# Kernel optimization log

Hardware: AMD Instinct MI355X
Metric: run time of the kernel (lower is better)

Reference implementation:

```python
import jax, jax.numpy as jnp
import numpy as np

N = 16384          # num_nodes
B = 2              # batch_size
F = 32             # feature_size (hard-coded in module)
G = 16             # num_gru_units
OUT = 16           # output_dim


def _normalized_laplacian(adj):
    # calculate_laplacian_with_self_loop: D^-1/2 (A + I) D^-1/2
    a = adj + jnp.eye(adj.shape[0], dtype=adj.dtype)
    d = a.sum(axis=1)
    dinv = jax.lax.rsqrt(d)
    return dinv[:, None] * a * dinv[None, :]


def setup_inputs() -> dict:
    key = jax.random.key(0)
    k1, k2, k3, k4 = jax.random.split(key, 4)
    adj = (jax.random.uniform(k1, (N, N), dtype=jnp.float32) < 0.01).astype(jnp.float32)
    laplacian = _normalized_laplacian(adj)
    inputs = jax.random.normal(k2, (B, N, F), dtype=jnp.float32)
    hidden_state = jax.random.normal(k3, (B, N * G), dtype=jnp.float32)
    # xavier_uniform for weights [(G+F), OUT]
    limit = np.sqrt(6.0 / (G + F + OUT)).astype(np.float32)
    weights = jax.random.uniform(k4, (G + F, OUT), dtype=jnp.float32, minval=-limit, maxval=limit)
    biases = jnp.zeros((OUT,), dtype=jnp.float32)
    return {"inputs": inputs, "hidden_state": hidden_state, "laplacian": laplacian,
            "weights": weights, "biases": biases}


def reference(inputs, hidden_state, laplacian, weights, biases):
    b, n, f = inputs.shape
    g = weights.shape[0] - f
    out_dim = weights.shape[1]
    h = hidden_state.reshape(b, n, g)
    cat = jnp.concatenate([inputs, h], axis=2)              # [B, N, F+G]
    # laplacian @ concat over the node dimension (same math as the
    # reshape/transpose dance + per-batch sparse GEMM loop in the original)
    ax = jnp.einsum('mn,bnc->bmc', laplacian, cat)          # [B, N, F+G]
    out = ax @ weights + biases                             # [B, N, OUT]
    return out.reshape(b, n * out_dim)
```

## Files before the change

### kernel.cpp

```cpp
#include <hip/hip_runtime.h>
#include <hip/hip_bf16.h>


#define NN   16384
#define FF   32
#define GG   16
#define OUTD 16
#define C96  96
#define BM   64
#define BK   64
#define SPLITK 2
#define KCHUNK (NN / SPLITK)
#define KITERS (KCHUNK / BK)

typedef __attribute__((ext_vector_type(8))) short short8;
typedef __attribute__((ext_vector_type(4))) float f32x4;

using as1_void = __attribute__((address_space(1))) void;
using as3_void = __attribute__((address_space(3))) void;

__device__ __forceinline__ unsigned short f2bf(float f) {
  __hip_bfloat16 h = __float2bfloat16(f);
  return __builtin_bit_cast(unsigned short, h);
}

__device__ __forceinline__ void wg_barrier() {
  asm volatile("" ::: "memory");
  __builtin_amdgcn_s_barrier();
  asm volatile("" ::: "memory");
}

__global__ __launch_bounds__(256) void prep_xt(const float* __restrict__ inp,
                                               const float* __restrict__ hid,
                                               unsigned short* __restrict__ xt) {
  __shared__ float lds_cat[C96][64];
  const int tid = threadIdx.x;
  const int n0 = blockIdx.x * 64;

#pragma unroll
  for (int r = 0; r < 2; ++r) {
    int fi = tid + r * 256;
    int n = fi >> 3;
    int f4 = fi & 7;
#pragma unroll
    for (int b = 0; b < 2; ++b) {
      const float4* src = (const float4*)(inp + ((size_t)b * NN + (n0 + n)) * FF) + f4;
      float4 v = *src;
      int c = b * 48 + f4 * 4;
      lds_cat[c + 0][n] = v.x;
      lds_cat[c + 1][n] = v.y;
      lds_cat[c + 2][n] = v.z;
      lds_cat[c + 3][n] = v.w;
    }
  }
  {
    int n = tid >> 2;
    int g4 = tid & 3;
#pragma unroll
    for (int b = 0; b < 2; ++b) {
      const float4* src = (const float4*)(hid + ((size_t)b * NN + (n0 + n)) * GG) + g4;
      float4 v = *src;
      int c = b * 48 + 32 + g4 * 4;
      lds_cat[c + 0][n] = v.x;
      lds_cat[c + 1][n] = v.y;
      lds_cat[c + 2][n] = v.z;
      lds_cat[c + 3][n] = v.w;
    }
  }
  __syncthreads();
#pragma unroll
  for (int r = 0; r < 3; ++r) {
    int u = tid + r * 256;
    int c = u >> 3;
    int nn = (u & 7) * 8;
    short8 o;
#pragma unroll
    for (int j = 0; j < 8; ++j) o[j] = (short)f2bf(lds_cat[c][nn + j]);
    *(short8*)(xt + (size_t)c * NN + n0 + nn) = o;
  }
}

__global__ __launch_bounds__(256, 2) void spmm_main(const float* __restrict__ L,
                                                    const unsigned short* __restrict__ xt,
                                                    float* __restrict__ cp) {
  __shared__ __align__(16) float lds_a[2][BM * BK];
  __shared__ __align__(16) unsigned short lds_b[2][C96 * BK];

  const int tid = threadIdx.x;
  const int wave = tid >> 6;
  const int lane = tid & 63;

  const int wg = blockIdx.x;
  const int swz = (wg & 7) * (512 / 8) + (wg >> 3);
  const int my = swz >> 8;
  const int mx = swz & 255;
  const int m0 = mx * BM;
  const int kbase = my * KCHUNK;

  const float* asrc[4];
  int adst[4];
#pragma unroll
  for (int a = 0; a < 4; ++a) {
    int s = wave * 256 + a * 64 + lane;
    int row = s >> 4;
    int cu = (s & 15) ^ (row & 15);
    asrc[a] = L + (size_t)(m0 + row) * NN + kbase + cu * 4;
    adst[a] = (wave * 256 + a * 64) * 4;
  }
  const unsigned short* bsrc[3];
  int bdst[3];
#pragma unroll
  for (int bi = 0; bi < 3; ++bi) {
    int s = wave * 192 + bi * 64 + lane;
    int c = s >> 3;
    int kg = (s & 7) ^ (c & 7);
    bsrc[bi] = xt + (size_t)c * NN + kbase + kg * 8;
    bdst[bi] = (wave * 192 + bi * 64) * 8;
  }

  const int rowA = wave * 16 + (lane & 15);
  const int lq = lane >> 4;
  int aoff[2][2];
#pragma unroll
  for (int kk = 0; kk < 2; ++kk) {
    int cu0 = kk * 8 + lq * 2;
    aoff[kk][0] = (rowA * 16 + (cu0 ^ (rowA & 15))) * 4;
    aoff[kk][1] = (rowA * 16 + ((cu0 + 1) ^ (rowA & 15))) * 4;
  }
  int boff[2][6];
#pragma unroll
  for (int kk = 0; kk < 2; ++kk)
#pragma unroll
    for (int t = 0; t < 6; ++t) {
      int c = t * 16 + (lane & 15);
      int kg = kk * 4 + lq;
      boff[kk][t] = (c * 8 + (kg ^ (c & 7))) * 8;
    }

  f32x4 acc[6];
#pragma unroll
  for (int t = 0; t < 6; ++t) acc[t] = (f32x4){0.f, 0.f, 0.f, 0.f};

  auto stage = [&](int buf, int ko) {
#pragma unroll
    for (int a = 0; a < 4; ++a)
      __builtin_amdgcn_global_load_lds((const as1_void*)(asrc[a] + ko),
                                       (as3_void*)(&lds_a[buf][adst[a]]), 16, 0, 0);
#pragma unroll
    for (int bi = 0; bi < 3; ++bi)
      __builtin_amdgcn_global_load_lds((const as1_void*)(bsrc[bi] + ko),
                                       (as3_void*)(&lds_b[buf][bdst[bi]]), 16, 0, 0);
  };

  auto compute = [&](int buf) {
#pragma unroll
    for (int kk = 0; kk < 2; ++kk) {
      f32x4 a0 = *(const f32x4*)(&lds_a[buf][aoff[kk][0]]);
      f32x4 a1 = *(const f32x4*)(&lds_a[buf][aoff[kk][1]]);
      short8 af;
      af[0] = (short)f2bf(a0[0]);
      af[1] = (short)f2bf(a0[1]);
      af[2] = (short)f2bf(a0[2]);
      af[3] = (short)f2bf(a0[3]);
      af[4] = (short)f2bf(a1[0]);
      af[5] = (short)f2bf(a1[1]);
      af[6] = (short)f2bf(a1[2]);
      af[7] = (short)f2bf(a1[3]);
#pragma unroll
      for (int t = 0; t < 6; ++t) {
        short8 bf = *(const short8*)(&lds_b[buf][boff[kk][t]]);
        acc[t] = __builtin_amdgcn_mfma_f32_16x16x32_bf16(af, bf, acc[t], 0, 0, 0);
      }
    }
  };

  stage(0, 0);
  int cur = 0;
  for (int it = 0; it < KITERS - 1; ++it) {
    stage(cur ^ 1, (it + 1) * BK);
    asm volatile("s_waitcnt vmcnt(7)" ::: "memory");
    __builtin_amdgcn_s_barrier();
    asm volatile("" ::: "memory");
    compute(cur);
    wg_barrier();
    cur ^= 1;
  }
  asm volatile("s_waitcnt vmcnt(0)" ::: "memory");
  __builtin_amdgcn_s_barrier();
  asm volatile("" ::: "memory");
  compute(cur);

  float* cpd = cp + ((size_t)my * NN + m0) * C96;
#pragma unroll
  for (int t = 0; t < 6; ++t) {
    int col = t * 16 + (lane & 15);
#pragma unroll
    for (int r = 0; r < 4; ++r) {
      int row = wave * 16 + lq * 4 + r;
      cpd[(size_t)row * C96 + col] = acc[t][r];
    }
  }
}

__global__ __launch_bounds__(256) void epilogue(const float* __restrict__ cp,
                                                const float* __restrict__ w,
                                                const float* __restrict__ bias,
                                                float* __restrict__ out) {
  __shared__ float lds_c[64 * 97];
  __shared__ float lds_w[48 * 16];
  __shared__ float lds_bias[16];
  const int tid = threadIdx.x;
  const int n0 = blockIdx.x * 64;

  for (int i = tid; i < 768; i += 256) lds_w[i] = w[i];
  if (tid < 16) lds_bias[tid] = bias[tid];

  const size_t base = (size_t)n0 * C96;
#pragma unroll
  for (int i = 0; i < 24; ++i) {
    int e = tid + i * 256;
    float s = 0.f;
#pragma unroll
    for (int sp = 0; sp < SPLITK; ++sp)
      s += cp[(size_t)sp * (NN * C96) + base + e];
    lds_c[e + e / 96] = s;
  }
  __syncthreads();

  const int node = tid >> 2;
  const int b = (tid >> 1) & 1;
  const int o0 = (tid & 1) * 8;
  const float* crow = &lds_c[node * 97 + b * 48];
  float accv[8];
#pragma unroll
  for (int o = 0; o < 8; ++o) accv[o] = lds_bias[o0 + o];
#pragma unroll
  for (int j = 0; j < 48; ++j) {
    float cv = crow[j];
#pragma unroll
    for (int o = 0; o < 8; ++o) accv[o] += cv * lds_w[j * 16 + o0 + o];
  }
  size_t ob = (size_t)b * (NN * OUTD) + (size_t)(n0 + node) * OUTD + o0;
  float4 v0 = {accv[0], accv[1], accv[2], accv[3]};
  float4 v1 = {accv[4], accv[5], accv[6], accv[7]};
  *(float4*)(out + ob) = v0;
  *(float4*)(out + ob + 4) = v1;
}

extern "C" void kernel_launch(void* const* d_in, const int* in_sizes, int n_in,
                              void* d_out, int out_size, void* d_ws, size_t ws_size,
                              hipStream_t stream) {
  (void)in_sizes; (void)n_in; (void)out_size; (void)ws_size;
  const float* inp = (const float*)d_in[0];
  const float* hid = (const float*)d_in[1];
  const float* lap = (const float*)d_in[2];
  const float* wts = (const float*)d_in[3];
  const float* bia = (const float*)d_in[4];
  float* out = (float*)d_out;

  unsigned short* xt = (unsigned short*)d_ws;
  float* cp = (float*)((char*)d_ws + (4u << 20));

  prep_xt<<<NN / 64, 256, 0, stream>>>(inp, hid, xt);
  spmm_main<<<dim3(NN / BM * SPLITK), 256, 0, stream>>>(lap, xt, cp);
  epilogue<<<NN / 64, 256, 0, stream>>>(cp, wts, bia, out);
}
```

Measured before the change: 1.330 ms.

## Restructure spmm pipeline to read tiles into registers before issuing next prefetch

The main loop now copies each LDS tile into registers with inline ds_read_b128, waits, and barriers. It then issues the global-to-LDS prefetch for the tile two steps ahead into the buffer just freed, and runs the MFMAs from registers. This keeps two tiles of loads in flight while compute proceeds and drops the trailing barrier each iteration, with precomputed absolute LDS addresses and a loop unrolled by two. The cost is more registers for the staged fragments, which could hurt occupancy at the two-workgroup launch bound.

```diff
diff --git a/kernel.cpp b/kernel.cpp
--- a/kernel.cpp
+++ b/kernel.cpp
@@ -24,10 +24,19 @@
   return __builtin_bit_cast(unsigned short, h);
 }
 
-__device__ __forceinline__ void wg_barrier() {
-  asm volatile("" ::: "memory");
-  __builtin_amdgcn_s_barrier();
-  asm volatile("" ::: "memory");
+__device__ __forceinline__ unsigned lds_off(const void* p) {
+  return (unsigned)(uintptr_t)(as3_void*)p;
+}
+
+__device__ __forceinline__ f32x4 ds_read128f(unsigned addr) {
+  f32x4 r;
+  asm volatile("ds_read_b128 %0, %1" : "=v"(r) : "v"(addr));
+  return r;
+}
+__device__ __forceinline__ short8 ds_read128s(unsigned addr) {
+  short8 r;
+  asm volatile("ds_read_b128 %0, %1" : "=v"(r) : "v"(addr));
+  return r;
 }
 
 __global__ __launch_bounds__(256) void prep_xt(const float* __restrict__ inp,
@@ -83,8 +92,10 @@
 __global__ __launch_bounds__(256, 2) void spmm_main(const float* __restrict__ L,
                                                     const unsigned short* __restrict__ xt,
                                                     float* __restrict__ cp) {
-  __shared__ __align__(16) float lds_a[2][BM * BK];
-  __shared__ __align__(16) unsigned short lds_b[2][C96 * BK];
+  __shared__ __align__(16) float lds_a0[BM * BK];
+  __shared__ __align__(16) float lds_a1[BM * BK];
+  __shared__ __align__(16) unsigned short lds_b0[C96 * BK];
+  __shared__ __align__(16) unsigned short lds_b1[C96 * BK];
 
   const int tid = threadIdx.x;
   const int wave = tid >> 6;
@@ -120,75 +131,119 @@
 
   const int rowA = wave * 16 + (lane & 15);
   const int lq = lane >> 4;
-  int aoff[2][2];
+  const unsigned baA0 = lds_off(lds_a0), baA1 = lds_off(lds_a1);
+  const unsigned baB0 = lds_off(lds_b0), baB1 = lds_off(lds_b1);
+  unsigned aAdr[2][2][2];
+  unsigned bAdr[2][2][6];
 #pragma unroll
   for (int kk = 0; kk < 2; ++kk) {
-    int cu0 = kk * 8 + lq * 2;
-    aoff[kk][0] = (rowA * 16 + (cu0 ^ (rowA & 15))) * 4;
-    aoff[kk][1] = (rowA * 16 + ((cu0 + 1) ^ (rowA & 15))) * 4;
-  }
-  int boff[2][6];
-#pragma unroll
-  for (int kk = 0; kk < 2; ++kk)
+#pragma unroll
+    for (int j = 0; j < 2; ++j) {
+      int cu = (kk * 8 + lq * 2 + j) ^ (rowA & 15);
+      unsigned off = (unsigned)(rowA * 16 + cu) * 16u;
+      aAdr[0][kk][j] = baA0 + off;
+      aAdr[1][kk][j] = baA1 + off;
+    }
 #pragma unroll
     for (int t = 0; t < 6; ++t) {
       int c = t * 16 + (lane & 15);
-      int kg = kk * 4 + lq;
-      boff[kk][t] = (c * 8 + (kg ^ (c & 7))) * 8;
-    }
+      int kg = (kk * 4 + lq) ^ (c & 7);
+      unsigned off = (unsigned)(c * 8 + kg) * 16u;
+      bAdr[0][kk][t] = baB0 + off;
+      bAdr[1][kk][t] = baB1 + off;
+    }
+  }
 
   f32x4 acc[6];
 #pragma unroll
   for (int t = 0; t < 6; ++t) acc[t] = (f32x4){0.f, 0.f, 0.f, 0.f};
 
-  auto stage = [&](int buf, int ko) {
-#pragma unroll
-    for (int a = 0; a < 4; ++a)
-      __builtin_amdgcn_global_load_lds((const as1_void*)(asrc[a] + ko),
-                                       (as3_void*)(&lds_a[buf][adst[a]]), 16, 0, 0);
-#pragma unroll
-    for (int bi = 0; bi < 3; ++bi)
-      __builtin_amdgcn_global_load_lds((const as1_void*)(bsrc[bi] + ko),
-                                       (as3_void*)(&lds_b[buf][bdst[bi]]), 16, 0, 0);
-  };
-
-  auto compute = [&](int buf) {
-#pragma unroll
-    for (int kk = 0; kk < 2; ++kk) {
-      f32x4 a0 = *(const f32x4*)(&lds_a[buf][aoff[kk][0]]);
-      f32x4 a1 = *(const f32x4*)(&lds_a[buf][aoff[kk][1]]);
-      short8 af;
-      af[0] = (short)f2bf(a0[0]);
-      af[1] = (short)f2bf(a0[1]);
-      af[2] = (short)f2bf(a0[2]);
-      af[3] = (short)f2bf(a0[3]);
-      af[4] = (short)f2bf(a1[0]);
-      af[5] = (short)f2bf(a1[1]);
-      af[6] = (short)f2bf(a1[2]);
-      af[7] = (short)f2bf(a1[3]);
-#pragma unroll
-      for (int t = 0; t < 6; ++t) {
-        short8 bf = *(const short8*)(&lds_b[buf][boff[kk][t]]);
-        acc[t] = __builtin_amdgcn_mfma_f32_16x16x32_bf16(af, bf, acc[t], 0, 0, 0);
-      }
-    }
-  };
-
-  stage(0, 0);
-  int cur = 0;
-  for (int it = 0; it < KITERS - 1; ++it) {
-    stage(cur ^ 1, (it + 1) * BK);
+  f32x4 av[2][2];
+  short8 bv[2][6];
+
+#define STAGE7(Abuf, Bbuf, ko)                                                   \
+  do {                                                                           \
+    _Pragma("unroll")                                                            \
+    for (int a_ = 0; a_ < 4; ++a_)                                               \
+      __builtin_amdgcn_global_load_lds((const as1_void*)(asrc[a_] + (ko)),       \
+                                       (as3_void*)((Abuf) + adst[a_]), 16, 0, 0);\
+    _Pragma("unroll")                                                            \
+    for (int b_ = 0; b_ < 3; ++b_)                                               \
+      __builtin_amdgcn_global_load_lds((const as1_void*)(bsrc[b_] + (ko)),       \
+                                       (as3_void*)((Bbuf) + bdst[b_]), 16, 0, 0);\
+  } while (0)
+
+#define READ_TILE(BUF)                                                           \
+  do {                                                                           \
+    _Pragma("unroll")                                                            \
+    for (int kk_ = 0; kk_ < 2; ++kk_) {                                          \
+      av[kk_][0] = ds_read128f(aAdr[BUF][kk_][0]);                               \
+      av[kk_][1] = ds_read128f(aAdr[BUF][kk_][1]);                               \
+      _Pragma("unroll")                                                          \
+      for (int t_ = 0; t_ < 6; ++t_)                                             \
+        bv[kk_][t_] = ds_read128s(bAdr[BUF][kk_][t_]);                           \
+    }                                                                            \
+  } while (0)
+
+#define COMPUTE()                                                                \
+  do {                                                                           \
+    _Pragma("unroll")                                                            \
+    for (int kk_ = 0; kk_ < 2; ++kk_) {                                          \
+      f32x4 a0_ = av[kk_][0], a1_ = av[kk_][1];                                  \
+      short8 af_;                                                                \
+      af_[0] = (short)f2bf(a0_[0]); af_[1] = (short)f2bf(a0_[1]);                \
+      af_[2] = (short)f2bf(a0_[2]); af_[3] = (short)f2bf(a0_[3]);                \
+      af_[4] = (short)f2bf(a1_[0]); af_[5] = (short)f2bf(a1_[1]);                \
+      af_[6] = (short)f2bf(a1_[2]); af_[7] = (short)f2bf(a1_[3]);                \
+      _Pragma("unroll")                                                          \
+      for (int t_ = 0; t_ < 6; ++t_)                                             \
+        acc[t_] = __builtin_amdgcn_mfma_f32_16x16x32_bf16(af_, bv[kk_][t_],      \
+                                                          acc[t_], 0, 0, 0);     \
+    }                                                                            \
+  } while (0)
+
+#define TILE_BODY(BUF, Abuf, Bbuf, nextko)                                       \
+  do {                                                                           \
+    asm volatile("s_waitcnt vmcnt(7)" ::: "memory");                             \
+    __builtin_amdgcn_s_barrier();                                                \
+    READ_TILE(BUF);                                                              \
+    asm volatile("s_waitcnt lgkmcnt(0)" ::: "memory");                           \
+    __builtin_amdgcn_sched_barrier(0);                                           \
+    __builtin_amdgcn_s_barrier();                                                \
+    STAGE7(Abuf, Bbuf, (nextko));                                                \
+    __builtin_amdgcn_sched_barrier(0);                                           \
+    COMPUTE();                                                                   \
+  } while (0)
+
+  STAGE7(lds_a0, lds_b0, 0);
+  STAGE7(lds_a1, lds_b1, BK);
+
+  for (int p = 0; p < (KITERS - 2) / 2; ++p) {
+    const int t0 = 2 * p;
+    TILE_BODY(0, lds_a0, lds_b0, (t0 + 2) * BK);
+    TILE_BODY(1, lds_a1, lds_b1, (t0 + 3) * BK);
+  }
+
+  {
     asm volatile("s_waitcnt vmcnt(7)" ::: "memory");
     __builtin_amdgcn_s_barrier();
-    asm volatile("" ::: "memory");
-    compute(cur);
-    wg_barrier();
-    cur ^= 1;
-  }
-  asm volatile("s_waitcnt vmcnt(0)" ::: "memory");
-  __builtin_amdgcn_s_barrier();
-  asm volatile("" ::: "memory");
-  compute(cur);
+    READ_TILE(0);
+    asm volatile("s_waitcnt lgkmcnt(0)" ::: "memory");
+    __builtin_amdgcn_sched_barrier(0);
+    COMPUTE();
+
+    asm volatile("s_waitcnt vmcnt(0)" ::: "memory");
+    __builtin_amdgcn_s_barrier();
+    READ_TILE(1);
+    asm volatile("s_waitcnt lgkmcnt(0)" ::: "memory");
+    __builtin_amdgcn_sched_barrier(0);
+    COMPUTE();
+  }
+
+#undef TILE_BODY
+#undef COMPUTE
+#undef READ_TILE
+#undef STAGE7
 
   float* cpd = cp + ((size_t)my * NN + m0) * C96;
 #pragma unroll
```

Result: no change. 1.329 ms (-0.0%).
